# Kernel tuning notes

Measured on AMD Instinct MI355X. Metric: run time of the kernel, lower is better.

Reference implementation:

```python
import jax, jax.numpy as jnp
import numpy as np

B, C, H, W = 512, 64, 32, 64
NUM_NODE = 128


def setup_inputs() -> dict:
    key = jax.random.key(0)
    ks = jax.random.split(key, 11)
    f = jnp.float32
    def nrm(k, shape, s):
        return jax.random.normal(k, shape, f) * s
    return {
        "x":   jax.random.normal(ks[0], (B, C, H, W), f),
        "w11": nrm(ks[1], (32, 64, 1, 1), 0.1), "b11": nrm(ks[2], (32,), 0.05),
        "w12": nrm(ks[3], (16, 32, 3, 3), 0.1), "b12": nrm(ks[4], (16,), 0.05),
        "w21": nrm(ks[5], (8, 16, 1, 1), 0.1),  "b21": nrm(ks[6], (8,), 0.05),
        "w22": nrm(ks[7], (4, 8, 3, 3), 0.1),   "b22": nrm(ks[8], (4,), 0.05),
        "fcw": nrm(ks[9], (2 * NUM_NODE, 32 * 64 * 4), 0.05),
        "fcb": nrm(ks[10], (2 * NUM_NODE,), 0.05),
    }


def _conv_relu(x, w, b, pad):
    y = jax.lax.conv_general_dilated(
        x, w, window_strides=(1, 1), padding=[(pad, pad), (pad, pad)],
        dimension_numbers=("NCHW", "OIHW", "NCHW"))
    return jax.nn.relu(y + b[None, :, None, None])


def reference(x, w11, b11, w12, b12, w21, b21, w22, b22, fcw, fcb):
    # --- GraphGen3: conv stack -> fc -> n_Sigmoid -> [B, N, 2] ---
    h = _conv_relu(x, w11, b11, 0)
    h = _conv_relu(h, w12, b12, 1)
    h = _conv_relu(h, w21, b21, 0)
    h = _conv_relu(h, w22, b22, 1)          # [B, 4, 32, 64]
    z = h.reshape(h.shape[0], -1) @ fcw.T + fcb  # [B, 2N]
    c01 = jax.nn.sigmoid(3.0 * z).reshape(x.shape[0], -1, 2)  # n_Sigmoid(x, 3)
    # --- get_coord: scale normalized coords to pixel range ---
    Hd, Wd = x.shape[2], x.shape[3]
    coord = c01 * jnp.array([Hd - 1, Wd - 1], x.dtype)  # [B, N, 2]
    # --- th_batch_map_coordinates: clamp, corner gather, bilinear lerp ---
    ch = jnp.clip(coord[..., 0], 0.0, Hd - 1)
    cw = jnp.clip(coord[..., 1], 0.0, Wd - 1)
    h0 = jnp.floor(ch).astype(jnp.int32); h1 = jnp.ceil(ch).astype(jnp.int32)
    w0 = jnp.floor(cw).astype(jnp.int32); w1 = jnp.ceil(cw).astype(jnp.int32)
    bidx = jnp.arange(x.shape[0])[:, None]  # [B, 1]
    def gv(hi, wi):
        return x[bidx, :, hi, wi]           # gather -> [B, N, C]
    v_lt = gv(h0, w0); v_rt = gv(h1, w0)
    v_lb = gv(h0, w1); v_rb = gv(h1, w1)
    oh = (ch - h0.astype(x.dtype))[..., None]
    ow = (cw - w0.astype(x.dtype))[..., None]
    vt = v_lt + oh * (v_rt - v_lt)
    vb = v_lb + oh * (v_rb - v_lb)
    graph_feat = vt + ow * (vb - vt)        # [B, N, C] (matches permute(0,2,1))
    return graph_feat, coord
```

## Files before the change

### kernel.cpp

```cpp
#include <hip/hip_runtime.h>
#include <hip/hip_fp16.h>
#include <cstdint>

#define BATCH 512
#define CIN   64
#define HH    32
#define WW    64
#define HW    2048
#define C1    32
#define C2    16
#define C3    8
#define C4    4
#define NOUT  256
#define KFC   8192
#define NODES 128
#define KS    16
#define GF_SIZE (BATCH * NODES * CIN)

typedef __attribute__((ext_vector_type(8))) short bfrag;
typedef __attribute__((ext_vector_type(4))) float ffrag;

__device__ __forceinline__ ushort bf_trunc(float f) { return (ushort)(__float_as_uint(f) >> 16); }
__device__ __forceinline__ float  bf_truncf(float f) { return __uint_as_float(__float_as_uint(f) & 0xffff0000u); }
__device__ __forceinline__ ushort f2bf(float f) {
  uint32_t u = __float_as_uint(f);
  return (ushort)((u + 0x7fffu + ((u >> 16) & 1u)) >> 16);
}
__device__ __forceinline__ uint32_t pack2(float a, float b) {
  return (uint32_t)f2bf(a) | ((uint32_t)f2bf(b) << 16);
}
__device__ __forceinline__ uint32_t packhi2(float a, float b) {
  return (uint32_t)bf_trunc(a) | ((uint32_t)bf_trunc(b) << 16);
}
__device__ __forceinline__ ushort f2h(float f) { return __half_as_ushort(__float2half_rn(f)); }
__device__ __forceinline__ uint32_t packh2(float a, float b) {
  return (uint32_t)f2h(a) | ((uint32_t)f2h(b) << 16);
}
__device__ __forceinline__ float h2f(uint32_t u) { return __half2float(__ushort_as_half((ushort)u)); }

__device__ __forceinline__ bfrag ld_frag4(const uint32_t* tp) {
  union { uint32_t u[4]; bfrag b; } c;
  c.u[0] = tp[0]; c.u[1] = tp[1]; c.u[2] = tp[2]; c.u[3] = tp[3];
  return c.b;
}

__global__ __launch_bounds__(256) void k_front(
    const float* __restrict__ x, const float* __restrict__ w11, const float* __restrict__ b11,
    const float* __restrict__ fcw, ushort* __restrict__ fcwh, ushort* __restrict__ fcwl,
    ushort* __restrict__ h1g)
{
  if (blockIdx.y >= BATCH) {
    const int chunk = (blockIdx.y - BATCH) * 8 + blockIdx.x;
    const int i = (chunk * 256 + threadIdx.x) * 8;
    const float4 a = *(const float4*)(fcw + i);
    const float4 b = *(const float4*)(fcw + i + 4);
    uint4 hv, lv;
    hv.x = packhi2(a.x, a.y); hv.y = packhi2(a.z, a.w);
    hv.z = packhi2(b.x, b.y); hv.w = packhi2(b.z, b.w);
    lv.x = pack2(a.x - bf_truncf(a.x), a.y - bf_truncf(a.y));
    lv.y = pack2(a.z - bf_truncf(a.z), a.w - bf_truncf(a.w));
    lv.z = pack2(b.x - bf_truncf(b.x), b.y - bf_truncf(b.y));
    lv.w = pack2(b.z - bf_truncf(b.z), b.w - bf_truncf(b.w));
    *(uint4*)(fcwh + i) = hv;
    *(uint4*)(fcwl + i) = lv;
    return;
  }

  __shared__ uint32_t tb[256 * 33];
  const int t  = threadIdx.x;
  const int b  = blockIdx.y;
  const int rg = blockIdx.x;
  {
    const float* xp = x + (size_t)b * CIN * HW + rg * 256 + t;
    #pragma unroll
    for (int j = 0; j < 32; ++j) {
      float v0 = xp[(size_t)(2 * j) * HW];
      float v1 = xp[(size_t)(2 * j + 1) * HW];
      tb[t * 33 + j] = pack2(v0, v1);
    }
  }
  __syncthreads();

  const int l  = t & 63;
  const int wv = t >> 6;
  const int lr = l & 15;
  const int lg = l >> 4;
  bfrag w1h[2][2], w1l[2][2];
  #pragma unroll
  for (int m = 0; m < 2; ++m)
    #pragma unroll
    for (int ks = 0; ks < 2; ++ks) {
      const float* wp = w11 + (m * 16 + lr) * 64 + ks * 32 + lg * 8;
      #pragma unroll
      for (int e = 0; e < 8; ++e) {
        float v = wp[e];
        w1h[m][ks][e] = (short)bf_trunc(v);
        w1l[m][ks][e] = (short)f2bf(v - bf_truncf(v));
      }
    }
  float bias1[2][4];
  #pragma unroll
  for (int m = 0; m < 2; ++m)
    #pragma unroll
    for (int r = 0; r < 4; ++r) bias1[m][r] = b11[m * 16 + lg * 4 + r];

  #pragma unroll
  for (int i = 0; i < 4; ++i) {
    const int pxl = (wv * 4 + i) * 16 + lr;
    const bfrag f0 = ld_frag4(&tb[pxl * 33 + lg * 4]);
    const bfrag f1 = ld_frag4(&tb[pxl * 33 + 16 + lg * 4]);
    ffrag a0 = {0.f, 0.f, 0.f, 0.f}, a1 = {0.f, 0.f, 0.f, 0.f};
    a0 = __builtin_amdgcn_mfma_f32_16x16x32_bf16(w1h[0][0], f0, a0, 0, 0, 0);
    a0 = __builtin_amdgcn_mfma_f32_16x16x32_bf16(w1l[0][0], f0, a0, 0, 0, 0);
    a0 = __builtin_amdgcn_mfma_f32_16x16x32_bf16(w1h[0][1], f1, a0, 0, 0, 0);
    a0 = __builtin_amdgcn_mfma_f32_16x16x32_bf16(w1l[0][1], f1, a0, 0, 0, 0);
    a1 = __builtin_amdgcn_mfma_f32_16x16x32_bf16(w1h[1][0], f0, a1, 0, 0, 0);
    a1 = __builtin_amdgcn_mfma_f32_16x16x32_bf16(w1l[1][0], f0, a1, 0, 0, 0);
    a1 = __builtin_amdgcn_mfma_f32_16x16x32_bf16(w1h[1][1], f1, a1, 0, 0, 0);
    a1 = __builtin_amdgcn_mfma_f32_16x16x32_bf16(w1l[1][1], f1, a1, 0, 0, 0);
    ushort* hp = h1g + ((size_t)b * HW + rg * 256 + pxl) * C1;
    #pragma unroll
    for (int m = 0; m < 2; ++m) {
      float v0 = fmaxf((m ? a1[0] : a0[0]) + bias1[m][0], 0.f);
      float v1 = fmaxf((m ? a1[1] : a0[1]) + bias1[m][1], 0.f);
      float v2 = fmaxf((m ? a1[2] : a0[2]) + bias1[m][2], 0.f);
      float v3 = fmaxf((m ? a1[3] : a0[3]) + bias1[m][3], 0.f);
      *(uint2*)(hp + m * 16 + lg * 4) = uint2{pack2(v0, v1), pack2(v2, v3)};
    }
  }
}

__global__ __launch_bounds__(256) void k_conv234(
    const ushort* __restrict__ h1g, const float* __restrict__ w12, const float* __restrict__ b12,
    const float* __restrict__ w21, const float* __restrict__ b21,
    const float* __restrict__ w22, const float* __restrict__ b22,
    ushort* __restrict__ h4, int b0)
{
  __shared__ __align__(16) char smem[12 * 66 * 64];
  const int tid = threadIdx.x;
  const int l   = tid & 63;
  const int wv  = tid >> 6;
  const int lr  = l & 15;
  const int lg  = l >> 4;
  const int r0  = blockIdx.x * 8;
  const int bg  = b0 + blockIdx.y;

  if (tid < 192) {
    int row = tid >> 4, half = (tid >> 3) & 1, q = tid & 7;
    int cell = row * 66 + (half ? 65 : 0);
    *(uint2*)(smem + (cell << 6) + q * 8) = uint2{0u, 0u};
  }
  {
    const int px = tid >> 2, q = tid & 3;
    const int colb  = px + 1;
    const int chunk = q ^ ((colb >> 1) & 3);
    #pragma unroll
    for (int ry = 0; ry < 12; ++ry) {
      const int y = r0 - 2 + ry;
      uint4 v = uint4{0u, 0u, 0u, 0u};
      if (y >= 0 && y < HH)
        v = *(const uint4*)(h1g + ((size_t)bg * HW + y * WW + px) * C1 + q * 8);
      *(uint4*)(smem + ((ry * 66 + colb) << 6) + (chunk << 4)) = v;
    }
  }
  __syncthreads();

  bfrag w2h[9], w2l[9];
  #pragma unroll
  for (int t = 0; t < 9; ++t) {
    const float* wp = w12 + lr * 288 + t;
    #pragma unroll
    for (int e = 0; e < 8; ++e) {
      float v = wp[(lg * 8 + e) * 9];
      w2h[t][e] = (short)bf_trunc(v);
      w2l[t][e] = (short)f2bf(v - bf_truncf(v));
    }
  }
  float bias2[4];
  #pragma unroll
  for (int r = 0; r < 4; ++r) bias2[r] = b12[lg * 4 + r];

  uint32_t ph0[10], ph1[10];
  #pragma unroll
  for (int i = 0; i < 10; ++i) {
    const int nt   = wv * 10 + i;
    const int hryo = nt >> 2;
    const int col0 = (nt & 3) << 4;
    ffrag acc = {0.f, 0.f, 0.f, 0.f};
    #pragma unroll
    for (int ky = 0; ky < 3; ++ky) {
      const int row = hryo + ky;
      #pragma unroll
      for (int kx = 0; kx < 3; ++kx) {
        const int colb  = col0 + lr + kx;
        const int chunk = lg ^ ((colb >> 1) & 3);
        const bfrag hv = *(const bfrag*)(smem + ((row * 66 + colb) << 6) + (chunk << 4));
        acc = __builtin_amdgcn_mfma_f32_16x16x32_bf16(w2h[ky * 3 + kx], hv, acc, 0, 0, 0);
        acc = __builtin_amdgcn_mfma_f32_16x16x32_bf16(w2l[ky * 3 + kx], hv, acc, 0, 0, 0);
      }
    }
    ph0[i] = packh2(fmaxf(acc[0] + bias2[0], 0.f), fmaxf(acc[1] + bias2[1], 0.f));
    ph1[i] = packh2(fmaxf(acc[2] + bias2[2], 0.f), fmaxf(acc[3] + bias2[3], 0.f));
  }
  __syncthreads();
  #pragma unroll
  for (int i = 0; i < 10; ++i) {
    const int nt   = wv * 10 + i;
    const int hryo = nt >> 2;
    const int col  = ((nt & 3) << 4) + lr;
    *(uint2*)(smem + ((hryo * 64 + col) << 5) + lg * 8) = uint2{ph0[i], ph1[i]};
  }
  __syncthreads();

  float* h3b = (float*)(smem + 20480);
  for (int p = tid; p < 640; p += 256) {
    const int ry = p >> 6, wc = p & 63;
    const int y  = r0 - 1 + ry;
    float* hd = h3b + (ry * 64 + wc) * 9;
    if (y >= 0 && y < HH) {
      const uint4 ua = *(const uint4*)(smem + ((ry * 64 + wc) << 5));
      const uint4 ub = *(const uint4*)(smem + ((ry * 64 + wc) << 5) + 16);
      uint32_t uw[8] = {ua.x, ua.y, ua.z, ua.w, ub.x, ub.y, ub.z, ub.w};
      float xv[16];
      #pragma unroll
      for (int j = 0; j < 8; ++j) {
        xv[2*j]   = h2f(uw[j] & 0xffffu);
        xv[2*j+1] = h2f(uw[j] >> 16);
      }
      float acc[C3];
      #pragma unroll
      for (int o = 0; o < C3; ++o) acc[o] = b21[o];
      #pragma unroll
      for (int c = 0; c < 16; ++c) {
        float v = xv[c];
        #pragma unroll
        for (int o = 0; o < C3; ++o)
          acc[o] = fmaf(v, w21[o * 16 + c], acc[o]);
      }
      #pragma unroll
      for (int c = 0; c < C3; ++c) hd[c] = fmaxf(acc[c], 0.f);
    } else {
      #pragma unroll
      for (int c = 0; c < C3; ++c) hd[c] = 0.f;
    }
  }
  __syncthreads();

  for (int p = tid; p < 512; p += 256) {
    const int yl = p >> 6, wc = p & 63, ry = yl + 1;
    float acc[C4] = {b22[0], b22[1], b22[2], b22[3]};
    #pragma unroll
    for (int ky = 0; ky < 3; ++ky) {
      #pragma unroll
      for (int kx = 0; kx < 3; ++kx) {
        const int wcc = wc + kx - 1;
        if (wcc < 0 || wcc >= WW) continue;
        const float* hb = h3b + ((ry + ky - 1) * 64 + wcc) * 9;
        const int tap = ky * 3 + kx;
        #pragma unroll
        for (int c = 0; c < C3; ++c) {
          float v = hb[c];
          #pragma unroll
          for (int o = 0; o < C4; ++o)
            acc[o] = fmaf(v, w22[(o * 8 + c) * 9 + tap], acc[o]);
        }
      }
    }
    const size_t base = (size_t)blockIdx.y * KFC + (r0 + yl) * WW + wc;
    #pragma unroll
    for (int o = 0; o < C4; ++o)
      h4[base + (size_t)o * HW] = f2bf(fmaxf(acc[o], 0.f));
  }
}

__global__ __launch_bounds__(256) void k_fc(
    const ushort* __restrict__ Ap_, const ushort* __restrict__ Bhp,
    const ushort* __restrict__ Blp, float* __restrict__ zpart, int cb)
{
  const int tid = threadIdx.x;
  const int l   = tid & 63;
  const int wv  = tid >> 6;
  const int lr  = l & 15;
  const int lg  = l >> 4;
  const int m0  = blockIdx.x * 64 + (wv >> 1) * 32;
  const int n0  = blockIdx.y * 64 + (wv & 1) * 32;
  const int k0  = blockIdx.z * (KFC / KS);
  ffrag acc[2][2] = {};
  #pragma unroll 1
  for (int kc = 0; kc < (KFC / KS) / 32; ++kc) {
    const int k = k0 + kc * 32 + lg * 8;
    bfrag ah[2], bh[2], bl[2];
    #pragma unroll
    for (int t = 0; t < 2; ++t) {
      int m = m0 + t * 16 + lr; if (m >= cb) m = cb - 1;
      ah[t] = *(const bfrag*)(Ap_ + (size_t)m * KFC + k);
      bh[t] = *(const bfrag*)(Bhp + (size_t)(n0 + t * 16 + lr) * KFC + k);
      bl[t] = *(const bfrag*)(Blp + (size_t)(n0 + t * 16 + lr) * KFC + k);
    }
    #pragma unroll
    for (int mt = 0; mt < 2; ++mt)
      #pragma unroll
      for (int nt = 0; nt < 2; ++nt) {
        acc[mt][nt] = __builtin_amdgcn_mfma_f32_16x16x32_bf16(ah[mt], bh[nt], acc[mt][nt], 0, 0, 0);
        acc[mt][nt] = __builtin_amdgcn_mfma_f32_16x16x32_bf16(ah[mt], bl[nt], acc[mt][nt], 0, 0, 0);
      }
  }
  #pragma unroll
  for (int mt = 0; mt < 2; ++mt)
    #pragma unroll
    for (int r = 0; r < 4; ++r) {
      const int m = m0 + mt * 16 + lg * 4 + r;
      if (m < cb)
        #pragma unroll
        for (int nt = 0; nt < 2; ++nt)
          zpart[((size_t)blockIdx.z * cb + m) * NOUT + n0 + nt * 16 + lr] = acc[mt][nt][r];
    }
}

__global__ __launch_bounds__(256) void k_gather(
    const float* __restrict__ x, const float* __restrict__ zpart,
    const float* __restrict__ fcb, float* __restrict__ out, int cb, int b0)
{
  const int bid = blockIdx.x;
  int bl, g;
  if ((cb & 7) == 0) {
    const int xcd = bid & 7;
    const int j   = bid >> 3;
    g  = j & 31;
    bl = (j >> 5) * 8 + xcd;
  } else {
    bl = bid >> 5;
    g  = bid & 31;
  }
  const int node = g * 4 + (threadIdx.x >> 6);
  const int l    = threadIdx.x & 63;
  const int bg   = b0 + bl;

  float val = 0.f;
  if (l < 2 * KS) {
    const int kb = l >> 1, comp = l & 1;
    val = zpart[((size_t)kb * cb + bl) * NOUT + node * 2 + comp];
  }
  #pragma unroll
  for (int off = 2; off < 2 * KS; off <<= 1) val += __shfl_xor(val, off);
  const float z0 = __shfl(val, 0) + fcb[node * 2 + 0];
  const float z1 = __shfl(val, 1) + fcb[node * 2 + 1];
  const float ch = 31.f / (1.f + __expf(-3.f * z0));
  const float cw = 63.f / (1.f + __expf(-3.f * z1));

  if (l < 2)
    out[GF_SIZE + (((size_t)bg * NODES + node) << 1) + l] = l ? cw : ch;

  const float chv = fminf(fmaxf(ch, 0.f), 31.f);
  const float cwv = fminf(fmaxf(cw, 0.f), 63.f);
  const float fh = floorf(chv), fw = floorf(cwv);
  const int h0 = (int)fh, h1i = (int)ceilf(chv);
  const int w0 = (int)fw, w1i = (int)ceilf(cwv);
  const float oh = chv - fh, ow = cwv - fw;
  const float* xbp = x + ((size_t)bg * CIN + l) * HW;
  const float v_lt = xbp[h0 * WW + w0];
  const float v_rt = xbp[h1i * WW + w0];
  const float v_lb = xbp[h0 * WW + w1i];
  const float v_rb = xbp[h1i * WW + w1i];
  const float vt = v_lt + oh * (v_rt - v_lt);
  const float vb = v_lb + oh * (v_rb - v_lb);
  out[((size_t)bg * NODES + node) * CIN + l] = vt + ow * (vb - vt);
}

extern "C" void kernel_launch(void* const* d_in, const int* in_sizes, int n_in,
                              void* d_out, int out_size, void* d_ws, size_t ws_size,
                              hipStream_t stream)
{
  (void)in_sizes; (void)n_in; (void)out_size; (void)ws_size;
  const float* x   = (const float*)d_in[0];
  const float* w11 = (const float*)d_in[1];
  const float* b11 = (const float*)d_in[2];
  const float* w12 = (const float*)d_in[3];
  const float* b12 = (const float*)d_in[4];
  const float* w21 = (const float*)d_in[5];
  const float* b21 = (const float*)d_in[6];
  const float* w22 = (const float*)d_in[7];
  const float* b22 = (const float*)d_in[8];
  const float* fcw = (const float*)d_in[9];
  const float* fcb = (const float*)d_in[10];
  float* out = (float*)d_out;
  char* p = (char*)d_ws;

  ushort* h1v  = (ushort*)p;  p += (size_t)BATCH * HW * C1 * 2;
  ushort* h4v  = (ushort*)p;  p += (size_t)BATCH * KFC * 2;
  float*  zpv  = (float*)p;   p += (size_t)KS * BATCH * NOUT * 4;
  ushort* fcwh = (ushort*)p;  p += (size_t)NOUT * KFC * 2;
  ushort* fcwl = (ushort*)p;

  k_front<<<dim3(8, BATCH + 128), 256, 0, stream>>>(x, w11, b11, fcw, fcwh, fcwl, h1v);
  k_conv234<<<dim3(4, BATCH), 256, 0, stream>>>(h1v, w12, b12, w21, b21, w22, b22, h4v, 0);
  k_fc<<<dim3(BATCH / 64, 4, KS), 256, 0, stream>>>(h4v, fcwh, fcwl, zpv, BATCH);
  k_gather<<<dim3(BATCH * 32), 256, 0, stream>>>(x, zpv, fcb, out, BATCH, 0);
}
```

Measured before the change: 242.7 us.

## Write channel-last bf16 copy of x in front kernel for coalesced gather

The front kernel already packs x into shared memory as bf16 channel pairs per pixel. It now also writes that tile out as a channel-last (NHWC) bf16 copy of x to workspace. The gather kernel reads the four bilinear corners from this copy, so the 64 lanes of a node hit 64 contiguous channels instead of channel planes 8 KB apart. The cost is an extra 128 MB workspace write in the front kernel, plus bf16 rounding of the gathered features, which previously came from the exact fp32 input and may now fail a tight tolerance.

Result: faster. 213.1 us, median of 2 (-12.2%).

```diff
diff --git a/kernel.cpp b/kernel.cpp
--- a/kernel.cpp
+++ b/kernel.cpp
@@ -37,6 +37,7 @@
   return (uint32_t)f2h(a) | ((uint32_t)f2h(b) << 16);
 }
 __device__ __forceinline__ float h2f(uint32_t u) { return __half2float(__ushort_as_half((ushort)u)); }
+__device__ __forceinline__ float bf2f(ushort u) { return __uint_as_float(((uint32_t)u) << 16); }
 
 __device__ __forceinline__ bfrag ld_frag4(const uint32_t* tp) {
   union { uint32_t u[4]; bfrag b; } c;
@@ -47,7 +48,7 @@
 __global__ __launch_bounds__(256) void k_front(
     const float* __restrict__ x, const float* __restrict__ w11, const float* __restrict__ b11,
     const float* __restrict__ fcw, ushort* __restrict__ fcwh, ushort* __restrict__ fcwl,
-    ushort* __restrict__ h1g)
+    ushort* __restrict__ xt, ushort* __restrict__ h1g)
 {
   if (blockIdx.y >= BATCH) {
     const int chunk = (blockIdx.y - BATCH) * 8 + blockIdx.x;
@@ -80,6 +81,21 @@
     }
   }
   __syncthreads();
+
+  {
+    ushort* op = xt + ((size_t)b * HW + rg * 256) * CIN;
+    #pragma unroll
+    for (int k = 0; k < 8; ++k) {
+      const int u = k * 256 + t;
+      const int p = u >> 3, q = u & 7;
+      uint4 v;
+      v.x = tb[p * 33 + q * 4 + 0];
+      v.y = tb[p * 33 + q * 4 + 1];
+      v.z = tb[p * 33 + q * 4 + 2];
+      v.w = tb[p * 33 + q * 4 + 3];
+      *(uint4*)(op + (size_t)u * 8) = v;
+    }
+  }
 
   const int l  = t & 63;
   const int wv = t >> 6;
@@ -318,7 +334,7 @@
 }
 
 __global__ __launch_bounds__(256) void k_gather(
-    const float* __restrict__ x, const float* __restrict__ zpart,
+    const ushort* __restrict__ xt, const float* __restrict__ zpart,
     const float* __restrict__ fcb, float* __restrict__ out, int cb, int b0)
 {
   const int bid = blockIdx.x;
@@ -357,11 +373,11 @@
   const int h0 = (int)fh, h1i = (int)ceilf(chv);
   const int w0 = (int)fw, w1i = (int)ceilf(cwv);
   const float oh = chv - fh, ow = cwv - fw;
-  const float* xbp = x + ((size_t)bg * CIN + l) * HW;
-  const float v_lt = xbp[h0 * WW + w0];
-  const float v_rt = xbp[h1i * WW + w0];
-  const float v_lb = xbp[h0 * WW + w1i];
-  const float v_rb = xbp[h1i * WW + w1i];
+  const ushort* xbp = xt + (size_t)bg * HW * CIN + l;
+  const float v_lt = bf2f(xbp[(size_t)(h0 * WW + w0) * CIN]);
+  const float v_rt = bf2f(xbp[(size_t)(h1i * WW + w0) * CIN]);
+  const float v_lb = bf2f(xbp[(size_t)(h0 * WW + w1i) * CIN]);
+  const float v_rb = bf2f(xbp[(size_t)(h1i * WW + w1i) * CIN]);
   const float vt = v_lt + oh * (v_rt - v_lt);
   const float vb = v_lb + oh * (v_rb - v_lb);
   out[((size_t)bg * NODES + node) * CIN + l] = vt + ow * (vb - vt);
@@ -386,14 +402,17 @@
   float* out = (float*)d_out;
   char* p = (char*)d_ws;
 
+  ushort* xtv  = (ushort*)p;  p += (size_t)BATCH * HW * CIN * 2;
   ushort* h1v  = (ushort*)p;  p += (size_t)BATCH * HW * C1 * 2;
   ushort* h4v  = (ushort*)p;  p += (size_t)BATCH * KFC * 2;
   float*  zpv  = (float*)p;   p += (size_t)KS * BATCH * NOUT * 4;
   ushort* fcwh = (ushort*)p;  p += (size_t)NOUT * KFC * 2;
   ushort* fcwl = (ushort*)p;
 
-  k_front<<<dim3(8, BATCH + 128), 256, 0, stream>>>(x, w11, b11, fcw, fcwh, fcwl, h1v);
-  k_conv234<<<dim3(4, BATCH), 256, 0, stream>>>(h1v, w12, b12, w21, b21, w22, b22, h4v, 0);
+  k_front<<<dim3(8, BATCH + 128), 256, 0, stream>>>(x, w11, b11, fcw, fcwh, fcwl,
+                                                    xtv, h1v);
+  k_conv234<<<dim3(4, BATCH), 256, 0, stream>>>(h1v, w12, b12, w21, b21, w22, b22,
+                                                h4v, 0);
   k_fc<<<dim3(BATCH / 64, 4, KS), 256, 0, stream>>>(h4v, fcwh, fcwl, zpv, BATCH);
-  k_gather<<<dim3(BATCH * 32), 256, 0, stream>>>(x, zpv, fcb, out, BATCH, 0);
-}
+  k_gather<<<dim3(BATCH * 32), 256, 0, stream>>>(xtv, zpv, fcb, out, BATCH, 0);
+}
```
